# Kernel tuning notes

Hardware: AMD Instinct MI355X
Metric: run time of the kernel (lower is better)

## Reference

```python
import jax, jax.numpy as jnp
import numpy as np

N_NODES = 100000
IN_C, HID_C, OUT_C = 128, 128, 64
N_EDGES, N_POS, N_NEG = 1600000, 200000, 200000
BN_EPS = 1e-5


def setup_inputs() -> dict:
    key = jax.random.key(0)
    ks = jax.random.split(key, 24)
    s = 0.05
    inp = {
        'x': jax.random.normal(ks[0], (N_NODES, IN_C), jnp.float32),
        'edge_index': jax.random.randint(ks[1], (2, N_EDGES), 0, N_NODES, jnp.int64 if jax.config.jax_enable_x64 else jnp.int32),
        'pos_edge_index': jax.random.randint(ks[2], (2, N_POS), 0, N_NODES, jnp.int32),
        'neg_edge_index': jax.random.randint(ks[3], (2, N_NEG), 0, N_NODES, jnp.int32),
        # SAGEConv layer 1 (in->hid): lin_l (bias) on aggregated neighbors, lin_r (no bias) on root
        'Wl1': jax.random.normal(ks[4], (IN_C, HID_C), jnp.float32) * s,
        'bl1': jnp.zeros((HID_C,), jnp.float32),
        'Wr1': jax.random.normal(ks[5], (IN_C, HID_C), jnp.float32) * s,
        'g1': jnp.ones((HID_C,), jnp.float32),
        'b1': jnp.zeros((HID_C,), jnp.float32),
        # SAGEConv layer 2 (hid->hid)
        'Wl2': jax.random.normal(ks[6], (HID_C, HID_C), jnp.float32) * s,
        'bl2': jnp.zeros((HID_C,), jnp.float32),
        'Wr2': jax.random.normal(ks[7], (HID_C, HID_C), jnp.float32) * s,
        'g2': jnp.ones((HID_C,), jnp.float32),
        'b2': jnp.zeros((HID_C,), jnp.float32),
        # SAGEConv layer 3 (hid->out)
        'Wl3': jax.random.normal(ks[8], (HID_C, OUT_C), jnp.float32) * s,
        'bl3': jnp.zeros((OUT_C,), jnp.float32),
        'Wr3': jax.random.normal(ks[9], (HID_C, OUT_C), jnp.float32) * s,
        # edge predictor: Linear(2*out, hid) -> ReLU -> Linear(hid, 1)
        'We1': jax.random.normal(ks[10], (2 * OUT_C, HID_C), jnp.float32) * s,
        'be1': jnp.zeros((HID_C,), jnp.float32),
        'We2': jax.random.normal(ks[11], (HID_C, 1), jnp.float32) * s,
        'be2': jnp.zeros((1,), jnp.float32),
    }
    return inp


def _sage_conv(x, src, dst, Wl, bl, Wr):
    # mean aggregation of source features at destination nodes (PyG SAGEConv default)
    msg = x[src]                                                   # [E, C] gather
    agg = jax.ops.segment_sum(msg, dst, num_segments=N_NODES)      # [N, C] scatter-add
    deg = jax.ops.segment_sum(jnp.ones((src.shape[0],), x.dtype), dst, num_segments=N_NODES)
    mean = agg / jnp.maximum(deg, 1.0)[:, None]
    return mean @ Wl + bl + x @ Wr


def _bn_eval(x, gamma, beta):
    # BatchNorm1d eval mode with init running stats (mean 0, var 1)
    return x * (gamma / jnp.sqrt(1.0 + BN_EPS)) + beta


def _encode(x, edge_index, Wl1, bl1, Wr1, g1, b1, Wl2, bl2, Wr2, g2, b2, Wl3, bl3, Wr3):
    src, dst = edge_index[0], edge_index[1]
    h = x
    # layer 1 (+ residual: in_channels == hidden_channels)
    h1 = jax.nn.relu(_bn_eval(_sage_conv(h, src, dst, Wl1, bl1, Wr1), g1, b1))
    h = h1 + h if h.shape[1] == h1.shape[1] else h1
    # layer 2 (+ residual)
    h2 = jax.nn.relu(_bn_eval(_sage_conv(h, src, dst, Wl2, bl2, Wr2), g2, b2))
    h = h2 + h
    # output layer (no norm/relu/residual)
    return _sage_conv(h, src, dst, Wl3, bl3, Wr3)


def _decode(z, edge_index, We1, be1, We2, be2):
    s, d = edge_index[0], edge_index[1]
    ef = jnp.concatenate([z[s], z[d]], axis=-1)           # [E, 2*OUT_C]
    hidden = jax.nn.relu(ef @ We1 + be1)
    return jax.nn.sigmoid((hidden @ We2 + be2)[:, 0])


def reference(x, edge_index, pos_edge_index, neg_edge_index,
              Wl1, bl1, Wr1, g1, b1, Wl2, bl2, Wr2, g2, b2, Wl3, bl3, Wr3,
              We1, be1, We2, be2):
    z = _encode(x, edge_index, Wl1, bl1, Wr1, g1, b1, Wl2, bl2, Wr2, g2, b2, Wl3, bl3, Wr3)
    pos = _decode(z, pos_edge_index, We1, be1, We2, be2)
    neg = _decode(z, neg_edge_index, We1, be1, We2, be2)
    return (z, pos, neg)
```

## Files before the change

kernel.cpp:

```cpp
#include <hip/hip_runtime.h>
#include <hip/hip_bf16.h>

typedef unsigned short u16;
typedef unsigned char u8;
typedef short short8 __attribute__((ext_vector_type(8)));
typedef float floatx4 __attribute__((ext_vector_type(4)));
typedef float floatx2 __attribute__((ext_vector_type(2)));

__device__ __forceinline__ float b2f(u16 u) {
    unsigned v = ((unsigned)u) << 16;
    float f;
    __builtin_memcpy(&f, &v, 4);
    return f;
}
__device__ __forceinline__ float b2f_lo(unsigned w) { return b2f((u16)(w & 0xffffu)); }
__device__ __forceinline__ float b2f_hi(unsigned w) { return b2f((u16)(w >> 16)); }
__device__ __forceinline__ u16 f2b(float f) {
    unsigned u;
    __builtin_memcpy(&u, &f, 4);
    u = u + 0x7fffu + ((u >> 16) & 1u);
    return (u16)(u >> 16);
}
__device__ __forceinline__ unsigned pack2(float a, float b) {
    return (unsigned)f2b(a) | ((unsigned)f2b(b) << 16);
}
__device__ __forceinline__ float loadp(const void* p, int i, int f) {
    return f ? ((const float*)p)[i] : b2f(((const u16*)p)[i]);
}
__device__ __forceinline__ u8 f2e4m3(float v) {
    int r = __builtin_amdgcn_cvt_pk_fp8_f32(v, v, 0, false);
    return (u8)(r & 0xff);
}
__device__ __forceinline__ void acc16_fp8(float* a, uint4 p) {
    floatx2 f;
    f = __builtin_amdgcn_cvt_pk_f32_fp8((int)p.x, false); a[0] += f[0];  a[1] += f[1];
    f = __builtin_amdgcn_cvt_pk_f32_fp8((int)p.x, true);  a[2] += f[0];  a[3] += f[1];
    f = __builtin_amdgcn_cvt_pk_f32_fp8((int)p.y, false); a[4] += f[0];  a[5] += f[1];
    f = __builtin_amdgcn_cvt_pk_f32_fp8((int)p.y, true);  a[6] += f[0];  a[7] += f[1];
    f = __builtin_amdgcn_cvt_pk_f32_fp8((int)p.z, false); a[8] += f[0];  a[9] += f[1];
    f = __builtin_amdgcn_cvt_pk_f32_fp8((int)p.z, true);  a[10] += f[0]; a[11] += f[1];
    f = __builtin_amdgcn_cvt_pk_f32_fp8((int)p.w, false); a[12] += f[0]; a[13] += f[1];
    f = __builtin_amdgcn_cvt_pk_f32_fp8((int)p.w, true);  a[14] += f[0]; a[15] += f[1];
}

__global__ void sniff_kernel(const unsigned* __restrict__ xw, const int* __restrict__ eiw,
                             int* __restrict__ flags) {
    __shared__ int s_fp32, s_i64;
    if (threadIdx.x == 0) { s_fp32 = 0; s_i64 = 1; }
    __syncthreads();
    int t = threadIdx.x;
    unsigned w = xw[t];
    float lo = b2f_lo(w);
    if (!(fabsf(lo) <= 64.0f)) atomicOr(&s_fp32, 1);
    if (eiw[2 * t + 1] != 0) atomicAnd(&s_i64, 0);
    __syncthreads();
    if (t == 0) { flags[0] = s_fp32; flags[1] = s_i64; }
}

__global__ void cvt_x_kernel(const void* __restrict__ x, u16* __restrict__ xb,
                             u16* __restrict__ x8,
                             const int* __restrict__ flags, int nPairs) {
    int f = flags[0];
    int i = blockIdx.x * 256 + threadIdx.x;
    if (i >= nPairs) return;
    float lo, hi;
    if (f) {
        float2 v = ((const float2*)x)[i];
        lo = v.x; hi = v.y;
        ((unsigned*)xb)[i] = pack2(lo, hi);
    } else {
        unsigned w = ((const unsigned*)x)[i];
        lo = b2f_lo(w); hi = b2f_hi(w);
        ((unsigned*)xb)[i] = w;
    }
    int r = __builtin_amdgcn_cvt_pk_fp8_f32(lo, hi, 0, false);
    x8[i] = (u16)(r & 0xffff);
}

__global__ void prep_all_kernel(const void* Wl1, const void* Wr1, u16* __restrict__ Wcat1,
                                const void* Wl2, const void* Wr2, u16* __restrict__ Wcat2,
                                const void* Wl3, const void* Wr3, u16* __restrict__ Wcat3,
                                const void* We1, u16* __restrict__ Web,
                                const void* g1, const void* b1, const void* bl1,
                                float* __restrict__ al1, float* __restrict__ bt1,
                                const void* g2, const void* b2, const void* bl2,
                                float* __restrict__ al2, float* __restrict__ bt2,
                                const void* bl3,
                                float* __restrict__ al3, float* __restrict__ bt3,
                                const void* be1, const void* We2, const void* be2,
                                float* __restrict__ dparams,
                                const int* __restrict__ flags) {
    int f = flags[0];
    int idx = blockIdx.x * 256 + threadIdx.x;
    if (idx < 16384) {
        Wcat1[idx] = f ? f2b(((const float*)Wl1)[idx]) : ((const u16*)Wl1)[idx];
        Wcat1[16384 + idx] = f ? f2b(((const float*)Wr1)[idx]) : ((const u16*)Wr1)[idx];
    } else if (idx < 32768) {
        int i = idx - 16384;
        Wcat2[i] = f ? f2b(((const float*)Wl2)[i]) : ((const u16*)Wl2)[i];
        Wcat2[16384 + i] = f ? f2b(((const float*)Wr2)[i]) : ((const u16*)Wr2)[i];
    } else if (idx < 49152) {
        int i = idx - 32768;
        int k = i >> 7, n = i & 127;
        const void* src = (n < 64) ? Wl3 : Wr3;
        int j = k * 64 + (n & 63);
        Wcat3[i] = f ? f2b(((const float*)src)[j]) : ((const u16*)src)[j];
    } else if (idx < 65536) {
        int i = idx - 49152;
        Web[i] = f ? f2b(((const float*)We1)[i]) : ((const u16*)We1)[i];
    } else {
        int i = idx - 65536;
        if (i < 128) {
            float s = loadp(g1, i, f) * rsqrtf(1.0f + 1e-5f);
            al1[i] = s;
            bt1[i] = loadp(bl1, i, f) * s + loadp(b1, i, f);
        } else if (i < 256) {
            int j = i - 128;
            float s = loadp(g2, j, f) * rsqrtf(1.0f + 1e-5f);
            al2[j] = s;
            bt2[j] = loadp(bl2, j, f) * s + loadp(b2, j, f);
        } else if (i < 384) {
            int j = i - 256;
            al3[j] = 1.0f;
            bt3[j] = (j < 64) ? 0.0f : loadp(bl3, j - 64, f);
        } else if (i < 512) {
            int j = i - 384;
            dparams[j] = loadp(be1, j, f);
            dparams[128 + j] = loadp(We2, j, f);
            if (j == 0) dparams[256] = loadp(be2, 0, f);
        }
    }
}

__device__ __forceinline__ int edge_at(const int* ei, long long idx, int i64) {
    return i64 ? ei[2 * idx] : ei[idx];
}

__global__ __launch_bounds__(256) void bucket_count_kernel(const int* __restrict__ ei,
                                                           int* __restrict__ blockhist,
                                                           int E, int EPB, int B1, int nbuck,
                                                           const int* __restrict__ flags) {
    __shared__ int hist[1024];
    for (int i = threadIdx.x; i < nbuck; i += 256) hist[i] = 0;
    __syncthreads();
    int i64 = flags[1];
    int b = blockIdx.x;
    int lo = b * EPB, hi = min(lo + EPB, E);
    for (int e = lo + (int)threadIdx.x; e < hi; e += 256) {
        int d = edge_at(ei, (long long)E + e, i64);
        atomicAdd(&hist[d >> 7], 1);
    }
    __syncthreads();
    for (int k = threadIdx.x; k < nbuck; k += 256)
        blockhist[(size_t)k * B1 + b] = hist[k];
}

__global__ __launch_bounds__(64) void colscan_kernel(int* __restrict__ blockhist,
                                                     int* __restrict__ coltot, int B1) {
    int k = blockIdx.x, l = threadIdx.x;
    int* bh = blockhist + (size_t)k * B1;
    int x0 = (l < B1) ? bh[l] : 0;
    int x1 = (64 + l < B1) ? bh[64 + l] : 0;
    int s0 = x0;
    #pragma unroll
    for (int off = 1; off < 64; off <<= 1) {
        int u = __shfl_up(s0, off, 64);
        if (l >= off) s0 += u;
    }
    int tot0 = __shfl(s0, 63, 64);
    int s1 = x1;
    #pragma unroll
    for (int off = 1; off < 64; off <<= 1) {
        int u = __shfl_up(s1, off, 64);
        if (l >= off) s1 += u;
    }
    int tot1 = __shfl(s1, 63, 64);
    s1 += tot0;
    if (l < B1) bh[l] = s0 - x0;
    if (64 + l < B1) bh[64 + l] = s1 - x1;
    if (l == 0) coltot[k] = tot0 + tot1;
}

__global__ __launch_bounds__(1024) void base_scan_kernel(const int* __restrict__ coltot,
                                                         int* __restrict__ bucketbase,
                                                         int* __restrict__ rowptrN,
                                                         int nbuck, int E) {
    __shared__ int wsum[16];
    int t = threadIdx.x, lane = t & 63, w = t >> 6;
    int v = (t < nbuck) ? coltot[t] : 0;
    int inc = v;
    #pragma unroll
    for (int off = 1; off < 64; off <<= 1) {
        int u = __shfl_up(inc, off, 64);
        if (lane >= off) inc += u;
    }
    if (lane == 63) wsum[w] = inc;
    __syncthreads();
    int add = 0;
    for (int i = 0; i < w; ++i) add += wsum[i];
    if (t < nbuck) bucketbase[t] = add + inc - v;
    if (t == 0) rowptrN[0] = E;
}

__global__ __launch_bounds__(256) void bucket_scatter_kernel(const int* __restrict__ ei,
                                                             const int* __restrict__ bucketbase,
                                                             const int* __restrict__ blockhist,
                                                             int2* __restrict__ pairs,
                                                             int E, int EPB, int B1, int nbuck,
                                                             const int* __restrict__ flags) {
    __shared__ int off[1024];
    int b = blockIdx.x;
    for (int k = threadIdx.x; k < nbuck; k += 256)
        off[k] = bucketbase[k] + blockhist[(size_t)k * B1 + b];
    __syncthreads();
    int i64 = flags[1];
    int lo = b * EPB, hi = min(lo + EPB, E);
    for (int e = lo + (int)threadIdx.x; e < hi; e += 256) {
        int s = edge_at(ei, e, i64);
        int d = edge_at(ei, (long long)E + e, i64);
        int slot = atomicAdd(&off[d >> 7], 1);
        pairs[slot] = make_int2(s, d);
    }
}

__global__ __launch_bounds__(256) void bucket_csr_kernel(const int2* __restrict__ pairs,
                                                         const int* __restrict__ bucketbase,
                                                         const int* __restrict__ coltot,
                                                         int* __restrict__ rowptr,
                                                         int* __restrict__ col, int N) {
    __shared__ int srcs[4096];
    __shared__ unsigned char dl[4096];
    __shared__ int hist[128], cur[128];
    int k = blockIdx.x, tid = threadIdx.x;
    if (tid < 128) hist[tid] = 0;
    __syncthreads();
    int base = bucketbase[k], cnt = coltot[k];
    int staged = min(cnt, 4096);
    for (int i = tid; i < cnt; i += 256) {
        int2 pr = pairs[base + i];
        int j = pr.y & 127;
        atomicAdd(&hist[j], 1);
        if (i < 4096) { srcs[i] = pr.x; dl[i] = (unsigned char)j; }
    }
    __syncthreads();
    if (tid < 64) {
        int x0 = hist[tid], x1 = hist[64 + tid];
        int s0 = x0;
        #pragma unroll
        for (int off = 1; off < 64; off <<= 1) {
            int u = __shfl_up(s0, off, 64);
            if (tid >= off) s0 += u;
        }
        int tot0 = __shfl(s0, 63, 64);
        int s1 = x1;
        #pragma unroll
        for (int off = 1; off < 64; off <<= 1) {
            int u = __shfl_up(s1, off, 64);
            if (tid >= off) s1 += u;
        }
        s1 += tot0;
        cur[tid] = s0 - x0;
        cur[64 + tid] = s1 - x1;
    }
    __syncthreads();
    int node0 = k << 7;
    if (tid < 128 && node0 + tid < N) rowptr[node0 + tid] = base + cur[tid];
    __syncthreads();
    for (int i = tid; i < staged; i += 256) {
        int slot = base + atomicAdd(&cur[dl[i]], 1);
        col[slot] = srcs[i];
    }
    for (int i = 4096 + tid; i < cnt; i += 256) {
        int2 pr = pairs[base + i];
        int slot = base + atomicAdd(&cur[pr.y & 127], 1);
        col[slot] = pr.x;
    }
}

template <int CH>
__global__ __launch_bounds__(256) void aggregate_fp8_kernel(const u8* __restrict__ X8,
                                                            const int* __restrict__ rowptr,
                                                            const int* __restrict__ col,
                                                            u16* __restrict__ meanout, int N) {
    constexpr int LPR = CH / 16;
    constexpr int GPB = 256 / LPR;
    int t = threadIdx.x;
    int g = t / LPR;
    int o = t % LPR;
    int u = blockIdx.x * GPB + g;
    if (u >= N) return;
    const uint4* Xv = (const uint4*)X8;
    int beg = rowptr[u], end = rowptr[u + 1];
    float a[16];
    #pragma unroll
    for (int i = 0; i < 16; ++i) a[i] = 0.f;
    int e = beg;
    for (; e + 4 <= end; e += 4) {
        int c0 = col[e], c1 = col[e + 1], c2 = col[e + 2], c3 = col[e + 3];
        uint4 p0 = Xv[(size_t)c0 * LPR + o];
        uint4 p1 = Xv[(size_t)c1 * LPR + o];
        uint4 p2 = Xv[(size_t)c2 * LPR + o];
        uint4 p3 = Xv[(size_t)c3 * LPR + o];
        acc16_fp8(a, p0); acc16_fp8(a, p1); acc16_fp8(a, p2); acc16_fp8(a, p3);
    }
    for (; e < end; ++e) {
        uint4 p = Xv[(size_t)col[e] * LPR + o];
        acc16_fp8(a, p);
    }
    int deg = end - beg;
    float inv = (deg > 0) ? 1.0f / (float)deg : 0.0f;
    uint4 ov0, ov1;
    ov0.x = pack2(a[0] * inv, a[1] * inv);   ov0.y = pack2(a[2] * inv, a[3] * inv);
    ov0.z = pack2(a[4] * inv, a[5] * inv);   ov0.w = pack2(a[6] * inv, a[7] * inv);
    ov1.x = pack2(a[8] * inv, a[9] * inv);   ov1.y = pack2(a[10] * inv, a[11] * inv);
    ov1.z = pack2(a[12] * inv, a[13] * inv); ov1.w = pack2(a[14] * inv, a[15] * inv);
    uint4* mo = (uint4*)meanout;
    mo[(size_t)u * (CH / 8) + o * 2 + 0] = ov0;
    mo[(size_t)u * (CH / 8) + o * 2 + 1] = ov1;
}

__global__ __launch_bounds__(256) void agg_combine_kernel(const u8* __restrict__ T8,
                                                          const int* __restrict__ rowptr,
                                                          const int* __restrict__ col,
                                                          const u16* __restrict__ ubuf,
                                                          u16* __restrict__ zbuf,
                                                          void* __restrict__ dout,
                                                          int N, const int* __restrict__ flags) {
    constexpr int LPR = 4;
    constexpr int GPB = 64;
    int f = flags[0];
    int t = threadIdx.x;
    int g = t / LPR;
    int o = t % LPR;
    int u = blockIdx.x * GPB + g;
    if (u >= N) return;
    const uint4* Xv = (const uint4*)T8;
    int beg = rowptr[u], end = rowptr[u + 1];
    float a[16];
    #pragma unroll
    for (int i = 0; i < 16; ++i) a[i] = 0.f;
    int e = beg;
    for (; e + 4 <= end; e += 4) {
        int c0 = col[e], c1 = col[e + 1], c2 = col[e + 2], c3 = col[e + 3];
        uint4 p0 = Xv[(size_t)c0 * LPR + o];
        uint4 p1 = Xv[(size_t)c1 * LPR + o];
        uint4 p2 = Xv[(size_t)c2 * LPR + o];
        uint4 p3 = Xv[(size_t)c3 * LPR + o];
        acc16_fp8(a, p0); acc16_fp8(a, p1); acc16_fp8(a, p2); acc16_fp8(a, p3);
    }
    for (; e < end; ++e) {
        uint4 p = Xv[(size_t)col[e] * LPR + o];
        acc16_fp8(a, p);
    }
    int deg = end - beg;
    float inv = (deg > 0) ? 1.0f / (float)deg : 0.0f;
    const uint4* uv = (const uint4*)(ubuf + (size_t)u * 64 + o * 16);
    uint4 u0 = uv[0], u1 = uv[1];
    float z[16];
    z[0] = a[0] * inv + b2f_lo(u0.x);  z[1] = a[1] * inv + b2f_hi(u0.x);
    z[2] = a[2] * inv + b2f_lo(u0.y);  z[3] = a[3] * inv + b2f_hi(u0.y);
    z[4] = a[4] * inv + b2f_lo(u0.z);  z[5] = a[5] * inv + b2f_hi(u0.z);
    z[6] = a[6] * inv + b2f_lo(u0.w);  z[7] = a[7] * inv + b2f_hi(u0.w);
    z[8] = a[8] * inv + b2f_lo(u1.x);  z[9] = a[9] * inv + b2f_hi(u1.x);
    z[10] = a[10] * inv + b2f_lo(u1.y); z[11] = a[11] * inv + b2f_hi(u1.y);
    z[12] = a[12] * inv + b2f_lo(u1.z); z[13] = a[13] * inv + b2f_hi(u1.z);
    z[14] = a[14] * inv + b2f_lo(u1.w); z[15] = a[15] * inv + b2f_hi(u1.w);
    uint4 zv0, zv1;
    zv0.x = pack2(z[0], z[1]);   zv0.y = pack2(z[2], z[3]);
    zv0.z = pack2(z[4], z[5]);   zv0.w = pack2(z[6], z[7]);
    zv1.x = pack2(z[8], z[9]);   zv1.y = pack2(z[10], z[11]);
    zv1.z = pack2(z[12], z[13]); zv1.w = pack2(z[14], z[15]);
    uint4* zo = (uint4*)(zbuf + (size_t)u * 64 + o * 16);
    zo[0] = zv0; zo[1] = zv1;
    if (f) {
        float* fo = (float*)dout + (size_t)u * 64 + o * 16;
        #pragma unroll
        for (int i = 0; i < 16; ++i) fo[i] = z[i];
    } else {
        uint4* bo = (uint4*)((u16*)dout + (size_t)u * 64 + o * 16);
        bo[0] = zv0; bo[1] = zv1;
    }
}

#define LDSA 40
__global__ __launch_bounds__(256) void gemm_sage_kernel(
    const u16* __restrict__ A1, const u16* __restrict__ A2,
    const u16* __restrict__ W, int N,
    const float* __restrict__ alpha, const float* __restrict__ beta,
    int addRes, u16* __restrict__ out, int ldo, u16* __restrict__ outB,
    u8* __restrict__ out8, int ld8,
    int M, int K, int relu) {
    __shared__ u16 As[64 * LDSA];
    __shared__ u16 Wt[64 * LDSA];
    int tid = threadIdx.x;
    int mBase = blockIdx.x * 64, nBase = blockIdx.y * 64;
    int lane = tid & 63, w = tid >> 6;
    int wm = w >> 1, wn = w & 1;
    int q = lane >> 4, r = lane & 15;

    floatx4 acc[2][2];
    #pragma unroll
    for (int mi = 0; mi < 2; ++mi)
        #pragma unroll
        for (int ni = 0; ni < 2; ++ni)
            acc[mi][ni] = (floatx4){0.f, 0.f, 0.f, 0.f};

    for (int k0 = 0; k0 < K; k0 += 32) {
        const u16* Abase = (k0 < 128) ? (A1 + k0) : (A2 + (k0 - 128));
        {
            int row = tid >> 2, kc = (tid & 3) * 8;
            int gr = mBase + row;
            short8 v = (short8){0, 0, 0, 0, 0, 0, 0, 0};
            if (gr < M) v = *(const short8*)(Abase + (size_t)gr * 128 + kc);
            *(short8*)(&As[row * LDSA + kc]) = v;
        }
        {
            int kk = tid >> 3, nc = (tid & 7) * 8;
            short8 v = *(const short8*)(W + (size_t)(k0 + kk) * N + nBase + nc);
            #pragma unroll
            for (int j = 0; j < 8; ++j) Wt[(nc + j) * LDSA + kk] = ((u16*)&v)[j];
        }
        __syncthreads();
        short8 af[2], bfv[2];
        #pragma unroll
        for (int mi = 0; mi < 2; ++mi)
            af[mi] = *(const short8*)(&As[(wm * 32 + mi * 16 + r) * LDSA + q * 8]);
        #pragma unroll
        for (int ni = 0; ni < 2; ++ni)
            bfv[ni] = *(const short8*)(&Wt[(wn * 32 + ni * 16 + r) * LDSA + q * 8]);
        #pragma unroll
        for (int mi = 0; mi < 2; ++mi)
            #pragma unroll
            for (int ni = 0; ni < 2; ++ni)
                acc[mi][ni] = __builtin_amdgcn_mfma_f32_16x16x32_bf16(af[mi], bfv[ni], acc[mi][ni], 0, 0, 0);
        __syncthreads();
    }

    #pragma unroll
    for (int mi = 0; mi < 2; ++mi)
        #pragma unroll
        for (int ni = 0; ni < 2; ++ni) {
            int colv = nBase + wn * 32 + ni * 16 + r;
            float al = alpha[colv], be = beta[colv];
            #pragma unroll
            for (int r4 = 0; r4 < 4; ++r4) {
                int row = mBase + wm * 32 + mi * 16 + q * 4 + r4;
                if (row < M) {
                    float v = acc[mi][ni][r4] * al + be;
                    if (relu) v = fmaxf(v, 0.0f);
                    if (addRes) v += b2f(A2[(size_t)row * 128 + colv]);
                    if (outB) {
                        if (colv < 64) out8[(size_t)row * 64 + colv] = f2e4m3(v);
                        else outB[(size_t)row * 64 + (colv - 64)] = f2b(v);
                    } else {
                        out[(size_t)row * ldo + colv] = f2b(v);
                        if (out8) out8[(size_t)row * ld8 + colv] = f2e4m3(v);
                    }
                }
            }
        }
}

__global__ __launch_bounds__(256) void decode_kernel(
    const u16* __restrict__ z,
    const int* __restrict__ sidx, const int* __restrict__ didx,
    const u16* __restrict__ Web,
    const float* __restrict__ dparams,
    void* __restrict__ dout, long long outBase, int nE,
    const int* __restrict__ flags) {
    __shared__ u16 Wt[128 * 136];
    __shared__ u16 As[64 * 136];
    __shared__ float red[4][32];
    __shared__ float be1f[128], We2f[128];
    int tid = threadIdx.x;
    int f = flags[0];

    {
        int k = tid >> 1, nc0 = (tid & 1) * 64;
        #pragma unroll
        for (int c = 0; c < 8; ++c) {
            short8 v = *(const short8*)(Web + k * 128 + nc0 + c * 8);
            #pragma unroll
            for (int j = 0; j < 8; ++j) Wt[(nc0 + c * 8 + j) * 136 + k] = ((u16*)&v)[j];
        }
    }
    if (tid < 128) { be1f[tid] = dparams[tid]; We2f[tid] = dparams[128 + tid]; }

    int eBase = blockIdx.x * 64;
    {
        int row = tid >> 2, ch = tid & 3;
        int e = eBase + row;
        if (e >= nE) e = nE - 1;
        int node = (ch < 2) ? sidx[e] : didx[e];
        int off = (ch & 1) * 32;
        const short8* src = (const short8*)(z + (size_t)node * 64 + off);
        #pragma unroll
        for (int j = 0; j < 4; ++j)
            *(short8*)(&As[row * 136 + ch * 32 + j * 8]) = src[j];
    }
    __syncthreads();

    int lane = tid & 63, w = tid >> 6;
    int wm = w >> 1, wn = w & 1;
    int q = lane >> 4, r = lane & 15;
    floatx4 acc[2][4];
    #pragma unroll
    for (int mi = 0; mi < 2; ++mi)
        #pragma unroll
        for (int ni = 0; ni < 4; ++ni)
            acc[mi][ni] = (floatx4){0.f, 0.f, 0.f, 0.f};

    #pragma unroll
    for (int k0 = 0; k0 < 128; k0 += 32) {
        short8 af[2], bfv[4];
        #pragma unroll
        for (int mi = 0; mi < 2; ++mi)
            af[mi] = *(const short8*)(&As[(wm * 32 + mi * 16 + r) * 136 + k0 + q * 8]);
        #pragma unroll
        for (int ni = 0; ni < 4; ++ni)
            bfv[ni] = *(const short8*)(&Wt[(wn * 64 + ni * 16 + r) * 136 + k0 + q * 8]);
        #pragma unroll
        for (int mi = 0; mi < 2; ++mi)
            #pragma unroll
            for (int ni = 0; ni < 4; ++ni)
                acc[mi][ni] = __builtin_amdgcn_mfma_f32_16x16x32_bf16(af[mi], bfv[ni], acc[mi][ni], 0, 0, 0);
    }

    float part[2][4] = {{0.f, 0.f, 0.f, 0.f}, {0.f, 0.f, 0.f, 0.f}};
    #pragma unroll
    for (int mi = 0; mi < 2; ++mi)
        #pragma unroll
        for (int ni = 0; ni < 4; ++ni) {
            int colv = wn * 64 + ni * 16 + r;
            float bb = be1f[colv], mm = We2f[colv];
            #pragma unroll
            for (int r4 = 0; r4 < 4; ++r4) {
                float v = acc[mi][ni][r4] + bb;
                part[mi][r4] += fmaxf(v, 0.0f) * mm;
            }
        }
    #pragma unroll
    for (int mi = 0; mi < 2; ++mi)
        #pragma unroll
        for (int r4 = 0; r4 < 4; ++r4) {
            float v = part[mi][r4];
            v += __shfl_xor(v, 1, 64);
            v += __shfl_xor(v, 2, 64);
            v += __shfl_xor(v, 4, 64);
            v += __shfl_xor(v, 8, 64);
            part[mi][r4] = v;
        }
    if (r == 0) {
        #pragma unroll
        for (int mi = 0; mi < 2; ++mi)
            #pragma unroll
            for (int r4 = 0; r4 < 4; ++r4)
                red[w][mi * 16 + q * 4 + r4] = part[mi][r4];
    }
    __syncthreads();
    if (tid < 64) {
        int e = eBase + tid;
        if (e < nE) {
            int half = tid >> 5, loc = tid & 31;
            float s = red[half * 2 + 0][loc] + red[half * 2 + 1][loc] + dparams[256];
            float sg = 1.0f / (1.0f + expf(-s));
            if (f) ((float*)dout)[outBase + e] = sg;
            else   ((u16*)dout)[outBase + e] = f2b(sg);
        }
    }
}


extern "C" void kernel_launch(void* const* d_in, const int* in_sizes, int n_in,
                              void* d_out, int out_size, void* d_ws, size_t ws_size,
                              hipStream_t stream) {
    const void* x   = d_in[0];
    const int* ei   = (const int*)d_in[1];
    const int* pos  = (const int*)d_in[2];
    const int* neg  = (const int*)d_in[3];
    const void* Wl1 = d_in[4];
    const void* bl1 = d_in[5];
    const void* Wr1 = d_in[6];
    const void* g1  = d_in[7];
    const void* b1  = d_in[8];
    const void* Wl2 = d_in[9];
    const void* bl2 = d_in[10];
    const void* Wr2 = d_in[11];
    const void* g2  = d_in[12];
    const void* b2  = d_in[13];
    const void* Wl3 = d_in[14];
    const void* bl3 = d_in[15];
    const void* Wr3 = d_in[16];
    const void* We1 = d_in[17];
    const void* be1 = d_in[18];
    const void* We2 = d_in[19];
    const void* be2 = d_in[20];

    const int N = in_sizes[0] / 128;
    const int E = in_sizes[1] / 2;
    const int nPos = in_sizes[2] / 2;
    const int nNeg = in_sizes[3] / 2;
    const int nbuck = (N + 127) >> 7;
    const int EPB = (((E + 95) / 96) + 3) & ~3;
    const int B1 = (E + EPB - 1) / EPB;

    char* p = (char*)d_ws;
    auto alloc = [&](size_t bytes) -> void* {
        void* r = (void*)p;
        p += (bytes + 255) & ~(size_t)255;
        return r;
    };
    int*   flags     = (int*)alloc(64);
    int*   blockhist = (int*)alloc((size_t)nbuck * B1 * 4);
    int*   coltot    = (int*)alloc((size_t)nbuck * 4);
    int*   bucketbase= (int*)alloc((size_t)nbuck * 4);
    int*   rowptr    = (int*)alloc((size_t)(N + 1) * 4);
    int2*  pairs     = (int2*)alloc((size_t)E * 8);
    int*   colbuf    = (int*)alloc((size_t)E * 4);
    u16*   xb      = (u16*)alloc((size_t)N * 128 * 2);
    u16*   hbufA   = (u16*)alloc((size_t)N * 128 * 2);
    u16*   meanbuf = (u16*)alloc((size_t)N * 128 * 2);
    u8*    x8      = (u8*)alloc((size_t)N * 128);
    u8*    h8      = (u8*)alloc((size_t)N * 128);
    u8*    t8      = (u8*)alloc((size_t)N * 64);
    u16*   Wcat1   = (u16*)alloc((size_t)256 * 128 * 2);
    u16*   Wcat2   = (u16*)alloc((size_t)256 * 128 * 2);
    u16*   Wcat3   = (u16*)alloc((size_t)128 * 128 * 2);
    u16*   Web     = (u16*)alloc((size_t)128 * 128 * 2);
    float* al1 = (float*)alloc(128 * 4);
    float* bt1 = (float*)alloc(128 * 4);
    float* al2 = (float*)alloc(128 * 4);
    float* bt2 = (float*)alloc(128 * 4);
    float* al3 = (float*)alloc(128 * 4);
    float* bt3 = (float*)alloc(128 * 4);
    float* dparams = (float*)alloc(260 * 4);
    u16* hbufB = xb;
    u16* ubuf  = meanbuf + (size_t)N * 64;
    u16* zbuf  = hbufA + (size_t)N * 64;

    sniff_kernel<<<1, 256, 0, stream>>>((const unsigned*)x, ei, flags);
    bucket_count_kernel<<<B1, 256, 0, stream>>>(ei, blockhist, E, EPB, B1, nbuck, flags);
    colscan_kernel<<<nbuck, 64, 0, stream>>>(blockhist, coltot, B1);
    base_scan_kernel<<<1, 1024, 0, stream>>>(coltot, bucketbase, rowptr + N, nbuck, E);
    bucket_scatter_kernel<<<B1, 256, 0, stream>>>(ei, bucketbase, blockhist, pairs, E, EPB, B1, nbuck, flags);
    bucket_csr_kernel<<<nbuck, 256, 0, stream>>>(pairs, bucketbase, coltot, rowptr, colbuf, N);

    cvt_x_kernel<<<(N * 64 + 255) / 256, 256, 0, stream>>>(x, xb, (u16*)x8, flags, N * 64);
    prep_all_kernel<<<(66048 + 255) / 256, 256, 0, stream>>>(
        Wl1, Wr1, Wcat1, Wl2, Wr2, Wcat2, Wl3, Wr3, Wcat3, We1, Web,
        g1, b1, bl1, al1, bt1, g2, b2, bl2, al2, bt2, bl3, al3, bt3,
        be1, We2, be2, dparams, flags);

    dim3 gemmGrid2((N + 63) / 64, 2);

    aggregate_fp8_kernel<128><<<(N + 31) / 32, 256, 0, stream>>>(x8, rowptr, colbuf, meanbuf, N);
    gemm_sage_kernel<<<gemmGrid2, 256, 0, stream>>>(meanbuf, xb, Wcat1, 128, al1, bt1,
                                                    1, hbufA, 128, nullptr, h8, 128, N, 256, 1);
    aggregate_fp8_kernel<128><<<(N + 31) / 32, 256, 0, stream>>>(h8, rowptr, colbuf, meanbuf, N);
    gemm_sage_kernel<<<gemmGrid2, 256, 0, stream>>>(meanbuf, hbufA, Wcat2, 128, al2, bt2,
                                                    1, hbufB, 128, nullptr, nullptr, 0, N, 256, 1);
    gemm_sage_kernel<<<gemmGrid2, 256, 0, stream>>>(hbufB, hbufB, Wcat3, 128, al3, bt3,
                                                    0, nullptr, 0, ubuf, t8, 64, N, 128, 0);
    agg_combine_kernel<<<(N + 63) / 64, 256, 0, stream>>>(t8, rowptr, colbuf, ubuf, zbuf,
                                                          d_out, N, flags);

    long long posBase = (long long)N * 64;
    long long negBase = posBase + nPos;
    decode_kernel<<<(nPos + 63) / 64, 256, 0, stream>>>(zbuf, pos, pos + nPos, Web, dparams,
                                                        d_out, posBase, nPos, flags);
    decode_kernel<<<(nNeg + 63) / 64, 256, 0, stream>>>(zbuf, neg, neg + nNeg, Web, dparams,
                                                        d_out, negBase, nNeg, flags);
}
```

Before: 494.0 us.

## Pre-transpose weights and load MFMA fragments directly from global memory

The weight-prep kernel now writes all weight matrices in an N-major (transposed) bf16 layout. With that layout the SAGE GEMM drops its LDS staging, element-wise transpose and both barriers, and each wave loads A and B MFMA fragments straight from global memory in a fully unrolled, K-templated loop. The decode kernel likewise stops transposing We1 into shared memory per block and reads B fragments from the transposed global buffer. This removes per-block transpose and synchronisation cost, but each fragment load is now a separate uncached-by-LDS global access and may reduce data reuse within a block.

```diff
diff --git a/kernel.cpp b/kernel.cpp
--- a/kernel.cpp
+++ b/kernel.cpp
@@ -77,10 +77,10 @@
     x8[i] = (u16)(r & 0xffff);
 }
 
-__global__ void prep_all_kernel(const void* Wl1, const void* Wr1, u16* __restrict__ Wcat1,
-                                const void* Wl2, const void* Wr2, u16* __restrict__ Wcat2,
-                                const void* Wl3, const void* Wr3, u16* __restrict__ Wcat3,
-                                const void* We1, u16* __restrict__ Web,
+__global__ void prep_all_kernel(const void* Wl1, const void* Wr1, u16* __restrict__ W1t,
+                                const void* Wl2, const void* Wr2, u16* __restrict__ W2t,
+                                const void* Wl3, const void* Wr3, u16* __restrict__ W3t,
+                                const void* We1, u16* __restrict__ Webt,
                                 const void* g1, const void* b1, const void* bl1,
                                 float* __restrict__ al1, float* __restrict__ bt1,
                                 const void* g2, const void* b2, const void* bl2,
@@ -92,24 +92,30 @@
                                 const int* __restrict__ flags) {
     int f = flags[0];
     int idx = blockIdx.x * 256 + threadIdx.x;
-    if (idx < 16384) {
-        Wcat1[idx] = f ? f2b(((const float*)Wl1)[idx]) : ((const u16*)Wl1)[idx];
-        Wcat1[16384 + idx] = f ? f2b(((const float*)Wr1)[idx]) : ((const u16*)Wr1)[idx];
-    } else if (idx < 32768) {
-        int i = idx - 16384;
-        Wcat2[i] = f ? f2b(((const float*)Wl2)[i]) : ((const u16*)Wl2)[i];
-        Wcat2[16384 + i] = f ? f2b(((const float*)Wr2)[i]) : ((const u16*)Wr2)[i];
-    } else if (idx < 49152) {
+    if (idx < 32768) {
+        int n = idx >> 8, k = idx & 255;
+        const void* src = (k < 128) ? Wl1 : Wr1;
+        int j = (k & 127) * 128 + n;
+        W1t[idx] = f ? f2b(((const float*)src)[j]) : ((const u16*)src)[j];
+    } else if (idx < 65536) {
         int i = idx - 32768;
-        int k = i >> 7, n = i & 127;
+        int n = i >> 8, k = i & 255;
+        const void* src = (k < 128) ? Wl2 : Wr2;
+        int j = (k & 127) * 128 + n;
+        W2t[i] = f ? f2b(((const float*)src)[j]) : ((const u16*)src)[j];
+    } else if (idx < 81920) {
+        int i = idx - 65536;
+        int n = i >> 7, k = i & 127;
         const void* src = (n < 64) ? Wl3 : Wr3;
         int j = k * 64 + (n & 63);
-        Wcat3[i] = f ? f2b(((const float*)src)[j]) : ((const u16*)src)[j];
-    } else if (idx < 65536) {
-        int i = idx - 49152;
-        Web[i] = f ? f2b(((const float*)We1)[i]) : ((const u16*)We1)[i];
+        W3t[i] = f ? f2b(((const float*)src)[j]) : ((const u16*)src)[j];
+    } else if (idx < 98304) {
+        int i = idx - 81920;
+        int n = i >> 7, k = i & 127;
+        int j = k * 128 + n;
+        Webt[i] = f ? f2b(((const float*)We1)[j]) : ((const u16*)We1)[j];
     } else {
-        int i = idx - 65536;
+        int i = idx - 98304;
         if (i < 128) {
             float s = loadp(g1, i, f) * rsqrtf(1.0f + 1e-5f);
             al1[i] = s;
@@ -382,16 +388,14 @@
     }
 }
 
-#define LDSA 40
+template <int K>
 __global__ __launch_bounds__(256) void gemm_sage_kernel(
     const u16* __restrict__ A1, const u16* __restrict__ A2,
-    const u16* __restrict__ W, int N,
+    const u16* __restrict__ Wt,
     const float* __restrict__ alpha, const float* __restrict__ beta,
     int addRes, u16* __restrict__ out, int ldo, u16* __restrict__ outB,
     u8* __restrict__ out8, int ld8,
-    int M, int K, int relu) {
-    __shared__ u16 As[64 * LDSA];
-    __shared__ u16 Wt[64 * LDSA];
+    int M, int relu) {
     int tid = threadIdx.x;
     int mBase = blockIdx.x * 64, nBase = blockIdx.y * 64;
     int lane = tid & 63, w = tid >> 6;
@@ -405,35 +409,22 @@
         for (int ni = 0; ni < 2; ++ni)
             acc[mi][ni] = (floatx4){0.f, 0.f, 0.f, 0.f};
 
+    int row0 = mBase + wm * 32 + r;
+    int row1 = row0 + 16;
+    int r0c = min(row0, M - 1), r1c = min(row1, M - 1);
+    const u16* bp = Wt + (size_t)(nBase + wn * 32 + r) * K + q * 8;
+
+    #pragma unroll
     for (int k0 = 0; k0 < K; k0 += 32) {
         const u16* Abase = (k0 < 128) ? (A1 + k0) : (A2 + (k0 - 128));
-        {
-            int row = tid >> 2, kc = (tid & 3) * 8;
-            int gr = mBase + row;
-            short8 v = (short8){0, 0, 0, 0, 0, 0, 0, 0};
-            if (gr < M) v = *(const short8*)(Abase + (size_t)gr * 128 + kc);
-            *(short8*)(&As[row * LDSA + kc]) = v;
-        }
-        {
-            int kk = tid >> 3, nc = (tid & 7) * 8;
-            short8 v = *(const short8*)(W + (size_t)(k0 + kk) * N + nBase + nc);
-            #pragma unroll
-            for (int j = 0; j < 8; ++j) Wt[(nc + j) * LDSA + kk] = ((u16*)&v)[j];
-        }
-        __syncthreads();
-        short8 af[2], bfv[2];
-        #pragma unroll
-        for (int mi = 0; mi < 2; ++mi)
-            af[mi] = *(const short8*)(&As[(wm * 32 + mi * 16 + r) * LDSA + q * 8]);
-        #pragma unroll
-        for (int ni = 0; ni < 2; ++ni)
-            bfv[ni] = *(const short8*)(&Wt[(wn * 32 + ni * 16 + r) * LDSA + q * 8]);
-        #pragma unroll
-        for (int mi = 0; mi < 2; ++mi)
-            #pragma unroll
-            for (int ni = 0; ni < 2; ++ni)
-                acc[mi][ni] = __builtin_amdgcn_mfma_f32_16x16x32_bf16(af[mi], bfv[ni], acc[mi][ni], 0, 0, 0);
-        __syncthreads();
+        short8 af0 = *(const short8*)(Abase + (size_t)r0c * 128 + q * 8);
+        short8 af1 = *(const short8*)(Abase + (size_t)r1c * 128 + q * 8);
+        short8 bf0 = *(const short8*)(bp + k0);
+        short8 bf1 = *(const short8*)(bp + 16 * K + k0);
+        acc[0][0] = __builtin_amdgcn_mfma_f32_16x16x32_bf16(af0, bf0, acc[0][0], 0, 0, 0);
+        acc[0][1] = __builtin_amdgcn_mfma_f32_16x16x32_bf16(af0, bf1, acc[0][1], 0, 0, 0);
+        acc[1][0] = __builtin_amdgcn_mfma_f32_16x16x32_bf16(af1, bf0, acc[1][0], 0, 0, 0);
+        acc[1][1] = __builtin_amdgcn_mfma_f32_16x16x32_bf16(af1, bf1, acc[1][1], 0, 0, 0);
     }
 
     #pragma unroll
@@ -464,26 +455,16 @@
 __global__ __launch_bounds__(256) void decode_kernel(
     const u16* __restrict__ z,
     const int* __restrict__ sidx, const int* __restrict__ didx,
-    const u16* __restrict__ Web,
+    const u16* __restrict__ Webt,
     const float* __restrict__ dparams,
     void* __restrict__ dout, long long outBase, int nE,
     const int* __restrict__ flags) {
-    __shared__ u16 Wt[128 * 136];
     __shared__ u16 As[64 * 136];
     __shared__ float red[4][32];
     __shared__ float be1f[128], We2f[128];
     int tid = threadIdx.x;
     int f = flags[0];
 
-    {
-        int k = tid >> 1, nc0 = (tid & 1) * 64;
-        #pragma unroll
-        for (int c = 0; c < 8; ++c) {
-            short8 v = *(const short8*)(Web + k * 128 + nc0 + c * 8);
-            #pragma unroll
-            for (int j = 0; j < 8; ++j) Wt[(nc0 + c * 8 + j) * 136 + k] = ((u16*)&v)[j];
-        }
-    }
     if (tid < 128) { be1f[tid] = dparams[tid]; We2f[tid] = dparams[128 + tid]; }
 
     int eBase = blockIdx.x * 64;
@@ -510,6 +491,7 @@
         for (int ni = 0; ni < 4; ++ni)
             acc[mi][ni] = (floatx4){0.f, 0.f, 0.f, 0.f};
 
+    const u16* bp = Webt + (size_t)(wn * 64 + r) * 128 + q * 8;
     #pragma unroll
     for (int k0 = 0; k0 < 128; k0 += 32) {
         short8 af[2], bfv[4];
@@ -518,7 +500,7 @@
             af[mi] = *(const short8*)(&As[(wm * 32 + mi * 16 + r) * 136 + k0 + q * 8]);
         #pragma unroll
         for (int ni = 0; ni < 4; ++ni)
-            bfv[ni] = *(const short8*)(&Wt[(wn * 64 + ni * 16 + r) * 136 + k0 + q * 8]);
+            bfv[ni] = *(const short8*)(bp + (size_t)ni * 16 * 128 + k0);
         #pragma unroll
         for (int mi = 0; mi < 2; ++mi)
             #pragma unroll
@@ -623,10 +605,10 @@
     u8*    x8      = (u8*)alloc((size_t)N * 128);
     u8*    h8      = (u8*)alloc((size_t)N * 128);
     u8*    t8      = (u8*)alloc((size_t)N * 64);
-    u16*   Wcat1   = (u16*)alloc((size_t)256 * 128 * 2);
-    u16*   Wcat2   = (u16*)alloc((size_t)256 * 128 * 2);
-    u16*   Wcat3   = (u16*)alloc((size_t)128 * 128 * 2);
-    u16*   Web     = (u16*)alloc((size_t)128 * 128 * 2);
+    u16*   W1t     = (u16*)alloc((size_t)128 * 256 * 2);
+    u16*   W2t     = (u16*)alloc((size_t)128 * 256 * 2);
+    u16*   W3t     = (u16*)alloc((size_t)128 * 128 * 2);
+    u16*   Webt    = (u16*)alloc((size_t)128 * 128 * 2);
     float* al1 = (float*)alloc(128 * 4);
     float* bt1 = (float*)alloc(128 * 4);
     float* al2 = (float*)alloc(128 * 4);
@@ -646,28 +628,28 @@
     bucket_csr_kernel<<<nbuck, 256, 0, stream>>>(pairs, bucketbase, coltot, rowptr, colbuf, N);
 
     cvt_x_kernel<<<(N * 64 + 255) / 256, 256, 0, stream>>>(x, xb, (u16*)x8, flags, N * 64);
-    prep_all_kernel<<<(66048 + 255) / 256, 256, 0, stream>>>(
-        Wl1, Wr1, Wcat1, Wl2, Wr2, Wcat2, Wl3, Wr3, Wcat3, We1, Web,
+    prep_all_kernel<<<(98816 + 255) / 256, 256, 0, stream>>>(
+        Wl1, Wr1, W1t, Wl2, Wr2, W2t, Wl3, Wr3, W3t, We1, Webt,
         g1, b1, bl1, al1, bt1, g2, b2, bl2, al2, bt2, bl3, al3, bt3,
         be1, We2, be2, dparams, flags);
 
     dim3 gemmGrid2((N + 63) / 64, 2);
 
     aggregate_fp8_kernel<128><<<(N + 31) / 32, 256, 0, stream>>>(x8, rowptr, colbuf, meanbuf, N);
-    gemm_sage_kernel<<<gemmGrid2, 256, 0, stream>>>(meanbuf, xb, Wcat1, 128, al1, bt1,
-                                                    1, hbufA, 128, nullptr, h8, 128, N, 256, 1);
+    gemm_sage_kernel<256><<<gemmGrid2, 256, 0, stream>>>(meanbuf, xb, W1t, al1, bt1,
+                                                         1, hbufA, 128, nullptr, h8, 128, N, 1);
     aggregate_fp8_kernel<128><<<(N + 31) / 32, 256, 0, stream>>>(h8, rowptr, colbuf, meanbuf, N);
-    gemm_sage_kernel<<<gemmGrid2, 256, 0, stream>>>(meanbuf, hbufA, Wcat2, 128, al2, bt2,
-                                                    1, hbufB, 128, nullptr, nullptr, 0, N, 256, 1);
-    gemm_sage_kernel<<<gemmGrid2, 256, 0, stream>>>(hbufB, hbufB, Wcat3, 128, al3, bt3,
-                                                    0, nullptr, 0, ubuf, t8, 64, N, 128, 0);
+    gemm_sage_kernel<256><<<gemmGrid2, 256, 0, stream>>>(meanbuf, hbufA, W2t, al2, bt2,
+                                                         1, hbufB, 128, nullptr, nullptr, 0, N, 1);
+    gemm_sage_kernel<128><<<gemmGrid2, 256, 0, stream>>>(hbufB, hbufB, W3t, al3, bt3,
+                                                         0, nullptr, 0, ubuf, t8, 64, N, 0);
     agg_combine_kernel<<<(N + 63) / 64, 256, 0, stream>>>(t8, rowptr, colbuf, ubuf, zbuf,
                                                           d_out, N, flags);
 
     long long posBase = (long long)N * 64;
     long long negBase = posBase + nPos;
-    decode_kernel<<<(nPos + 63) / 64, 256, 0, stream>>>(zbuf, pos, pos + nPos, Web, dparams,
+    decode_kernel<<<(nPos + 63) / 64, 256, 0, stream>>>(zbuf, pos, pos + nPos, Webt, dparams,
                                                         d_out, posBase, nPos, flags);
-    decode_kernel<<<(nNeg + 63) / 64, 256, 0, stream>>>(zbuf, neg, neg + nNeg, Web, dparams,
+    decode_kernel<<<(nNeg + 63) / 64, 256, 0, stream>>>(zbuf, neg, neg + nNeg, Webt, dparams,
                                                         d_out, negBase, nNeg, flags);
 }
```

Result: slower. 550.9 us (+11.5%).
